# Optimization experiments

Hardware: AMD Instinct MI355X
Metric: run time of the kernel (lower is better)

The kernel has to match this reference:

```python
import jax, jax.numpy as jnp
import numpy as np

NUM_ROUTING = 3
EPS = 1e-7  # keras.backend.epsilon()


def squash(x, axis=-1):
    # squash(s) = (||s||^2 / (1 + ||s||^2)) * s / ||s||, stabilized
    n2 = jnp.sum(x * x, axis=axis, keepdims=True)
    return (n2 / (1.0 + n2)) * x / jnp.sqrt(n2 + EPS)


def setup_inputs() -> dict:
    key = jax.random.key(0)
    k1, k2 = jax.random.split(key)
    B, N_IN, N_OUT, D = 32, 2048, 64, 16
    inputs = jax.random.normal(k1, (B, N_IN, N_OUT, D), dtype=jnp.float32)
    bias = jax.random.normal(k2, (N_OUT, D), dtype=jnp.float32) * 0.01
    return {"inputs": inputs, "bias": bias}


def reference(inputs, bias):
    # inputs: [b, n_in, n_out, d_out]; bias: [n_out, d_out]
    priors = jnp.zeros_like(inputs)
    outputs = None
    for i in range(NUM_ROUTING):
        agreements = jax.nn.softmax(priors, axis=2)           # over n_out
        outputs = jnp.sum(inputs * agreements, axis=1, keepdims=True)  # [b,1,n_out,d]
        outputs = squash(outputs + bias)                       # activation='linear' -> plain squash
        if i < NUM_ROUTING - 1:
            # agreement update, broadcast over d_out
            priors = priors + jnp.sum(inputs * outputs, axis=-1, keepdims=True)
    # reduce '... n_in n_out d_out -> ... n_out d_out' (n_in axis has size 1 here)
    return jnp.sum(outputs, axis=1)
```

## Files before the change

### kernel.cpp

```cpp
#include <hip/hip_runtime.h>
#include <math.h>

#define BB 32
#define NIN 2048
#define NOUT 64
#define DD 16
#define CH 16
#define RPC 128
#define TPB 512

typedef float    f4 __attribute__((ext_vector_type(4)));
typedef float    f8 __attribute__((ext_vector_type(8)));
typedef _Float16 h4 __attribute__((ext_vector_type(4)));
typedef _Float16 h8 __attribute__((ext_vector_type(8)));

__global__ __launch_bounds__(TPB, 2) void pass0_kernel(
    const float* __restrict__ x, h4* __restrict__ xh, f4* __restrict__ pout)
{
    const int blk  = blockIdx.x;
    const int chunk = blk & (CH - 1);
    const int b    = blk >> 4;
    const int tid  = threadIdx.x;
    const int lane = tid & 63, wave = tid >> 6;

    f4 acc[4];
    #pragma unroll
    for (int j = 0; j < 4; ++j) acc[j] = f4{0.f, 0.f, 0.f, 0.f};

    const size_t row0 = (size_t)b * NIN + (size_t)chunk * RPC;

    for (int r = wave; r < RPC; r += 8) {
        const f4* rp = (const f4*)x + (row0 + r) * 256;
        h4* hp = xh + (row0 + r) * 256;
        #pragma unroll
        for (int j = 0; j < 4; ++j) {
            f4 xv = __builtin_nontemporal_load(&rp[j * 64 + lane]);
            acc[j] += xv;
            hp[j * 64 + lane] = __builtin_convertvector(xv, h4);
        }
    }

    __shared__ f4 red[8][256];
    #pragma unroll
    for (int j = 0; j < 4; ++j) red[wave][j * 64 + lane] = acc[j];
    __syncthreads();
    if (tid < 256) {
        f4 s = red[0][tid];
        #pragma unroll
        for (int w = 1; w < 8; ++w) s += red[w][tid];
        pout[((size_t)(b * CH + chunk)) * 256 + tid] = s;
    }
}

__device__ __forceinline__ void compute_v(
    const f4* __restrict__ pin, const float* __restrict__ bias,
    int b, int tid, float scale, float* vsm, float* vout, int dowrite)
{
    if (tid < 256) {
        f4 s = pin[((size_t)b * CH) * 256 + tid];
        #pragma unroll
        for (int c = 1; c < CH; ++c) s += pin[((size_t)(b * CH + c)) * 256 + tid];
        const f4 bi = ((const f4*)bias)[tid];
        s = s * scale + bi;
        float n2 = s.x * s.x + s.y * s.y + s.z * s.z + s.w * s.w;
        n2 += __shfl_xor(n2, 1);
        n2 += __shfl_xor(n2, 2);
        const float k = n2 / ((1.0f + n2) * sqrtf(n2 + 1e-7f));
        const f4 v = s * k;
        *(f4*)(vsm + tid * 4) = v;
        if (dowrite) ((f4*)vout)[b * 256 + tid] = v;
    }
    __syncthreads();
}

template <int MODE>
__global__ __launch_bounds__(TPB, 2) void pass_kernel(
    const h8* __restrict__ xh,
    const f4* __restrict__ pin,
    const float* __restrict__ bias,
    const float* __restrict__ v0g,
    float* __restrict__ v0out,
    f4* __restrict__ pout)
{
    const int blk  = blockIdx.x;
    const int chunk = blk & (CH - 1);
    const int b    = blk >> 4;
    const int tid  = threadIdx.x;
    const int lane = tid & 63, wave = tid >> 6;

    __shared__ __align__(32) float vsm[1024];
    __shared__ __align__(32) float wsm[1024];
    __shared__ f4 red[8][256];

    if (MODE == 1) {
        compute_v(pin, bias, b, tid, 1.0f / 64.0f, vsm, v0out, chunk == 0);
    } else {
        if (tid < 256) *(f4*)(vsm + tid * 4) = ((const f4*)v0g)[b * 256 + tid];
        compute_v(pin, bias, b, tid, 1.0f, wsm, nullptr, 0);
    }

    f8 vaf[2], vbf[2];
    #pragma unroll
    for (int j = 0; j < 2; ++j) {
        const int idx = j * 64 + lane;
        vaf[j] = *(const f8*)(vsm + idx * 8);
        if (MODE == 2) vbf[j] = *(const f8*)(wsm + idx * 8);
    }

    f8 acc0 = {0.f, 0.f, 0.f, 0.f, 0.f, 0.f, 0.f, 0.f};
    f8 acc1 = acc0;
    const size_t row0 = (size_t)b * NIN + (size_t)chunk * RPC;

    #pragma unroll 2
    for (int r = wave; r < RPC; r += 8) {
        const h8* hp = xh + (row0 + r) * 128;
        const h8 hx0 = hp[lane];
        const h8 hx1 = hp[64 + lane];
        const f8 x0 = __builtin_convertvector(hx0, f8);
        const f8 x1 = __builtin_convertvector(hx1, f8);

        float d0 = 0.f, d1 = 0.f;
        #pragma unroll
        for (int k = 0; k < 8; ++k) d0 = fmaf(x0[k], vaf[0][k], d0);
        #pragma unroll
        for (int k = 0; k < 8; ++k) d1 = fmaf(x1[k], vaf[1][k], d1);
        if (MODE == 2) {
            #pragma unroll
            for (int k = 0; k < 8; ++k) d0 = fmaf(x0[k], vbf[0][k], d0);
            #pragma unroll
            for (int k = 0; k < 8; ++k) d1 = fmaf(x1[k], vbf[1][k], d1);
        }
        d0 += __shfl_xor(d0, 1);
        d1 += __shfl_xor(d1, 1);

        float m = fmaxf(d0, d1);
        #pragma unroll
        for (int o = 2; o <= 32; o <<= 1) m = fmaxf(m, __shfl_xor(m, o));
        const float e0 = __expf(d0 - m), e1 = __expf(d1 - m);
        float p = e0 + e1;
        #pragma unroll
        for (int o = 2; o <= 32; o <<= 1) p += __shfl_xor(p, o);
        const float inv = __builtin_amdgcn_rcpf(p);
        const float a0 = e0 * inv, a1 = e1 * inv;
        #pragma unroll
        for (int k = 0; k < 8; ++k) acc0[k] = fmaf(x0[k], a0, acc0[k]);
        #pragma unroll
        for (int k = 0; k < 8; ++k) acc1[k] = fmaf(x1[k], a1, acc1[k]);
    }

    *(f8*)(&red[wave][lane * 2])       = acc0;
    *(f8*)(&red[wave][128 + lane * 2]) = acc1;
    __syncthreads();
    if (tid < 256) {
        f4 s = red[0][tid];
        #pragma unroll
        for (int w = 1; w < 8; ++w) s += red[w][tid];
        pout[((size_t)(b * CH + chunk)) * 256 + tid] = s;
    }
}

__global__ __launch_bounds__(256) void finish_kernel(
    const f4* __restrict__ pin, const float* __restrict__ bias, f4* __restrict__ out)
{
    const int b = blockIdx.x;
    const int tid = threadIdx.x;
    f4 s = pin[((size_t)b * CH) * 256 + tid];
    #pragma unroll
    for (int c = 1; c < CH; ++c) s += pin[((size_t)(b * CH + c)) * 256 + tid];
    s = s + ((const f4*)bias)[tid];
    float n2 = s.x * s.x + s.y * s.y + s.z * s.z + s.w * s.w;
    n2 += __shfl_xor(n2, 1);
    n2 += __shfl_xor(n2, 2);
    const float k = n2 / ((1.0f + n2) * sqrtf(n2 + 1e-7f));
    out[b * 256 + tid] = s * k;
}

extern "C" void kernel_launch(void* const* d_in, const int* in_sizes, int n_in,
                              void* d_out, int out_size, void* d_ws, size_t ws_size,
                              hipStream_t stream) {
    const float* x    = (const float*)d_in[0];
    const float* bias = (const float*)d_in[1];
    float* out        = (float*)d_out;

    const size_t XH_BYTES = (size_t)BB * NIN * 1024 * 2;
    h4*    xh = (h4*)d_ws;
    float* pA = (float*)((char*)d_ws + XH_BYTES);
    float* pB = pA + (size_t)BB * CH * 1024;
    float* pC = pB + (size_t)BB * CH * 1024;
    float* v0buf = pC + (size_t)BB * CH * 1024;

    pass0_kernel<<<BB * CH, TPB, 0, stream>>>(x, xh, (f4*)pA);
    pass_kernel<1><<<BB * CH, TPB, 0, stream>>>((const h8*)xh, (const f4*)pA, bias,
                                                nullptr, v0buf, (f4*)pB);
    pass_kernel<2><<<BB * CH, TPB, 0, stream>>>((const h8*)xh, (const f4*)pB, bias,
                                                v0buf, nullptr, (f4*)pC);
    finish_kernel<<<BB, 256, 0, stream>>>((const f4*)pC, bias, (f4*)out);
}
```

Measured before the change: 117.7 us.

## Merge routing vectors, drop softmax max, prefetch rows, raise occupancy

Several changes land together. In mode 2 the two squashed output vectors are summed once, so each row needs one dot product instead of two, and dot8 uses a tree reduction to shorten dependency chains. The softmax max-subtraction and its shuffle reduction are removed, on the assumption that the logits stay small enough not to overflow exp. The next row's half-precision data is loaded one iteration ahead, and both kernels raise their launch-bounds occupancy hint from 2 to 4 blocks per CU, which limits registers and LDS per block.

After: 116.4 us (median of 2 runs). Within noise of the previous version (-1.1%).

```diff
diff --git a/kernel.cpp b/kernel.cpp
--- a/kernel.cpp
+++ b/kernel.cpp
@@ -14,7 +14,15 @@
 typedef _Float16 h4 __attribute__((ext_vector_type(4)));
 typedef _Float16 h8 __attribute__((ext_vector_type(8)));
 
-__global__ __launch_bounds__(TPB, 2) void pass0_kernel(
+__device__ __forceinline__ float dot8(f8 a, f8 b) {
+    float s01 = fmaf(a[1], b[1], a[0] * b[0]);
+    float s23 = fmaf(a[3], b[3], a[2] * b[2]);
+    float s45 = fmaf(a[5], b[5], a[4] * b[4]);
+    float s67 = fmaf(a[7], b[7], a[6] * b[6]);
+    return (s01 + s23) + (s45 + s67);
+}
+
+__global__ __launch_bounds__(TPB, 4) void pass0_kernel(
     const float* __restrict__ x, h4* __restrict__ xh, f4* __restrict__ pout)
 {
     const int blk  = blockIdx.x;
@@ -29,6 +37,7 @@
 
     const size_t row0 = (size_t)b * NIN + (size_t)chunk * RPC;
 
+    #pragma unroll 2
     for (int r = wave; r < RPC; r += 8) {
         const f4* rp = (const f4*)x + (row0 + r) * 256;
         h4* hp = xh + (row0 + r) * 256;
@@ -74,7 +83,7 @@
 }
 
 template <int MODE>
-__global__ __launch_bounds__(TPB, 2) void pass_kernel(
+__global__ __launch_bounds__(TPB, 4) void pass_kernel(
     const h8* __restrict__ xh,
     const f4* __restrict__ pin,
     const float* __restrict__ bias,
@@ -92,6 +101,12 @@
     __shared__ __align__(32) float wsm[1024];
     __shared__ f4 red[8][256];
 
+    const size_t row0 = (size_t)b * NIN + (size_t)chunk * RPC;
+
+    const h8* hp0 = xh + (row0 + wave) * 128;
+    h8 hx0 = hp0[lane];
+    h8 hx1 = hp0[64 + lane];
+
     if (MODE == 1) {
         compute_v(pin, bias, b, tid, 1.0f / 64.0f, vsm, v0out, chunk == 0);
     } else {
@@ -99,44 +114,33 @@
         compute_v(pin, bias, b, tid, 1.0f, wsm, nullptr, 0);
     }
 
-    f8 vaf[2], vbf[2];
+    f8 vaf[2];
     #pragma unroll
     for (int j = 0; j < 2; ++j) {
         const int idx = j * 64 + lane;
         vaf[j] = *(const f8*)(vsm + idx * 8);
-        if (MODE == 2) vbf[j] = *(const f8*)(wsm + idx * 8);
+        if (MODE == 2) vaf[j] += *(const f8*)(wsm + idx * 8);
     }
 
     f8 acc0 = {0.f, 0.f, 0.f, 0.f, 0.f, 0.f, 0.f, 0.f};
     f8 acc1 = acc0;
-    const size_t row0 = (size_t)b * NIN + (size_t)chunk * RPC;
 
     #pragma unroll 2
     for (int r = wave; r < RPC; r += 8) {
-        const h8* hp = xh + (row0 + r) * 128;
-        const h8 hx0 = hp[lane];
-        const h8 hx1 = hp[64 + lane];
         const f8 x0 = __builtin_convertvector(hx0, f8);
         const f8 x1 = __builtin_convertvector(hx1, f8);
-
-        float d0 = 0.f, d1 = 0.f;
-        #pragma unroll
-        for (int k = 0; k < 8; ++k) d0 = fmaf(x0[k], vaf[0][k], d0);
-        #pragma unroll
-        for (int k = 0; k < 8; ++k) d1 = fmaf(x1[k], vaf[1][k], d1);
-        if (MODE == 2) {
-            #pragma unroll
-            for (int k = 0; k < 8; ++k) d0 = fmaf(x0[k], vbf[0][k], d0);
-            #pragma unroll
-            for (int k = 0; k < 8; ++k) d1 = fmaf(x1[k], vbf[1][k], d1);
+        if (r + 8 < RPC) {
+            const h8* np = xh + (row0 + r + 8) * 128;
+            hx0 = np[lane];
+            hx1 = np[64 + lane];
         }
+
+        float d0 = dot8(x0, vaf[0]);
+        float d1 = dot8(x1, vaf[1]);
         d0 += __shfl_xor(d0, 1);
         d1 += __shfl_xor(d1, 1);
 
-        float m = fmaxf(d0, d1);
-        #pragma unroll
-        for (int o = 2; o <= 32; o <<= 1) m = fmaxf(m, __shfl_xor(m, o));
-        const float e0 = __expf(d0 - m), e1 = __expf(d1 - m);
+        const float e0 = __expf(d0), e1 = __expf(d1);
         float p = e0 + e1;
         #pragma unroll
         for (int o = 2; o <= 32; o <<= 1) p += __shfl_xor(p, o);
```
